# Optimization experiments

Measured on AMD Instinct MI355X. Metric: run time of the kernel, lower is better.

The kernel has to match this reference:

```python
import jax, jax.numpy as jnp
import numpy as np

N = 10000        # nodes
E = 320000       # edges (avg degree 32)
K = 3            # TAGConv default hops
D_IN, D_H, D_OUT = 256, 128, 64


def setup_inputs() -> dict:
    key = jax.random.key(0)
    ks = jax.random.split(key, 12)
    def w(k, shape):
        # xavier-uniform-ish init
        fan_in, fan_out = shape[-2], shape[-1]
        lim = float(np.sqrt(6.0 / (fan_in + fan_out)))
        return jax.random.uniform(k, shape, jnp.float32, -lim, lim)
    return {
        "x": jax.random.normal(ks[0], (N, D_IN), dtype=jnp.float32),
        "edge_index": jax.random.randint(ks[1], (2, E), 0, N, dtype=jnp.int32),
        "W1": w(ks[2], (K + 1, D_IN, D_H)),  "b1": jnp.zeros((D_H,), jnp.float32),
        "W2": w(ks[3], (K + 1, D_H, D_H)),   "b2": jnp.zeros((D_H,), jnp.float32),
        "W3": w(ks[4], (K + 1, D_H, D_OUT)), "b3": jnp.zeros((D_OUT,), jnp.float32),
        "Wf": w(ks[5], (D_OUT, D_OUT)),      "bf": jnp.zeros((D_OUT,), jnp.float32),
        "Wd": w(ks[6], (D_OUT, D_OUT)),
    }


def _gcn_norm(src, dst, n_nodes):
    # TAGConv's gcn_norm without self-loops: D^-1/2 A D^-1/2 edge weights
    deg = jax.ops.segment_sum(jnp.ones(src.shape, jnp.float32), dst,
                              num_segments=n_nodes)
    dis = jnp.where(deg > 0, jax.lax.rsqrt(jnp.maximum(deg, 1.0)), 0.0)
    return dis[src] * dis[dst]  # [E]


def _tagconv(x, src, dst, norm, W, b):
    # out = sum_{k=0..K} (A_hat^k x) @ W[k] + b
    out = x @ W[0]
    h = x
    for k in range(1, W.shape[0]):
        # message = norm_e * h[src_e], aggregated at dst
        h = jax.ops.segment_sum(norm[:, None] * h[src], dst,
                                num_segments=x.shape[0])
        out = out + h @ W[k]
    return out + b


def reference(x, edge_index, W1, b1, W2, b2, W3, b3, Wf, bf, Wd):
    src, dst = edge_index[0], edge_index[1]
    norm = _gcn_norm(src, dst, x.shape[0])
    h = jax.nn.relu(_tagconv(x, src, dst, norm, W1, b1))
    h = jax.nn.relu(_tagconv(h, src, dst, norm, W2, b2))
    h = jax.nn.relu(_tagconv(h, src, dst, norm, W3, b3))
    z = h @ Wf + bf                     # [N, D_OUT]
    adj = (z @ Wd) @ z.T                # [N, N] bilinear decode
    return adj
```

## Files before the change

### kernel.cpp

```cpp
#include <hip/hip_runtime.h>
#include <hip/hip_bf16.h>
#include <cstdint>
#include <cstddef>


typedef __attribute__((ext_vector_type(8)))  short short8;
typedef __attribute__((ext_vector_type(4)))  float f32x4;
typedef __attribute__((ext_vector_type(16))) float f32x16;

static __device__ __forceinline__ ushort f2bf(float f) {
    __hip_bfloat16 h = __float2bfloat16(f);
    return *reinterpret_cast<const ushort*>(&h);
}
static __device__ __forceinline__ float bf2f(ushort u) {
    union { uint i; float f; } v; v.i = ((uint)u) << 16; return v.f;
}


__global__ void count_kernel(const int* __restrict__ dst, int* __restrict__ counts, int E) {
    int e = blockIdx.x * blockDim.x + threadIdx.x;
    if (e < E) atomicAdd(&counts[dst[e]], 1);
}

__global__ void scan_kernel(const int* __restrict__ counts, int* __restrict__ rowstart,
                            float* __restrict__ dis, int n) {
    __shared__ int sums[1024];
    int t = threadIdx.x;
    int chunk = (n + 1023) / 1024;
    int base = t * chunk;
    int s = 0;
    for (int i = 0; i < chunk; ++i) {
        int idx = base + i;
        if (idx < n) s += counts[idx];
    }
    sums[t] = s;
    __syncthreads();
    for (int off = 1; off < 1024; off <<= 1) {
        int v = (t >= off) ? sums[t - off] : 0;
        __syncthreads();
        sums[t] += v;
        __syncthreads();
    }
    int run = sums[t] - s;
    for (int i = 0; i < chunk; ++i) {
        int idx = base + i;
        if (idx < n) {
            rowstart[idx] = run;
            int c = counts[idx];
            dis[idx] = (c > 0) ? rsqrtf((float)c) : 0.f;
            run += c;
        }
    }
    if (t == 1023) rowstart[n] = sums[1023];
}

__global__ void csr_fill_kernel(const int* __restrict__ src, const int* __restrict__ dst,
                                const float* __restrict__ dis, const int* __restrict__ rowstart,
                                int* __restrict__ cursor, int* __restrict__ csr_src,
                                float* __restrict__ csr_w, int E) {
    int e = blockIdx.x * blockDim.x + threadIdx.x;
    if (e < E) {
        int d = dst[e];
        int s = src[e];
        int pos = rowstart[d] + atomicAdd(&cursor[d], 1);
        csr_src[pos] = s;
        csr_w[pos]   = dis[s] * dis[d];
    }
}

static __device__ __forceinline__ void prep_w_elem(const float* W, ushort* Wp,
                                                   int DIN, int DOUT, int i) {
    int hp  = i / (DIN * DOUT);
    int rem = i - hp * DIN * DOUT;
    int d   = rem / DOUT;
    int o   = rem - d * DOUT;
    Wp[(size_t)(hp * DOUT + o) * DIN + d] = f2bf(W[i]);
}
static __device__ __forceinline__ void prep_wt_elem(const float* W, ushort* Wt,
                                                    int K, int C, int i) {
    int k = i / C, c = i - k * C;
    Wt[(size_t)c * K + k] = f2bf(W[i]);
}

__global__ void prep_all_kernel(const float* __restrict__ x, ushort* __restrict__ xb, int nx,
                                const float* __restrict__ W1, ushort* __restrict__ Wp1,
                                const float* __restrict__ W2, ushort* __restrict__ Wp2,
                                const float* __restrict__ W3, ushort* __restrict__ Wp3,
                                const float* __restrict__ Wf, ushort* __restrict__ Wfb,
                                const float* __restrict__ Wd, ushort* __restrict__ Wdb) {
    const int n1 = 4 * 256 * 128, n2 = 4 * 128 * 128, n3 = 4 * 128 * 64, nf = 64 * 64;
    int i = blockIdx.x * blockDim.x + threadIdx.x;
    if (i < nx) { xb[i] = f2bf(x[i]); return; }
    i -= nx;
    if (i < n1) { prep_w_elem(W1, Wp1, 256, 128, i); return; }
    i -= n1;
    if (i < n2) { prep_w_elem(W2, Wp2, 128, 128, i); return; }
    i -= n2;
    if (i < n3) { prep_w_elem(W3, Wp3, 128, 64, i); return; }
    i -= n3;
    if (i < nf) { prep_wt_elem(Wf, Wfb, 64, 64, i); return; }
    i -= nf;
    if (i < nf) { prep_wt_elem(Wd, Wdb, 64, 64, i); return; }
}

template <int DIN, int DOUT>
__global__ __launch_bounds__(256) void proj_gemm_kernel(
        const ushort* __restrict__ A, const ushort* __restrict__ Wp,
        const float* __restrict__ bias, ushort* __restrict__ y, int M) {
    constexpr int NJ = DOUT / 16;
    int tid = threadIdx.x, wave = tid >> 6, lane = tid & 63;
    int lr = lane & 15, lk = lane >> 4;
    int r0 = blockIdx.x * 32;
    int ra0 = min(r0 + lr, M - 1);
    int ra1 = min(r0 + 16 + lr, M - 1);

    f32x4 acc[2][NJ];
    #pragma unroll
    for (int mi = 0; mi < 2; ++mi)
        #pragma unroll
        for (int nj = 0; nj < NJ; ++nj)
            acc[mi][nj] = (f32x4){0.f, 0.f, 0.f, 0.f};

    const ushort* a0p = A + (size_t)ra0 * DIN + lk * 8;
    const ushort* a1p = A + (size_t)ra1 * DIN + lk * 8;
    #pragma unroll
    for (int kc = 0; kc < DIN; kc += 32) {
        short8 a0 = *(const short8*)(a0p + kc);
        short8 a1 = *(const short8*)(a1p + kc);
        #pragma unroll
        for (int nj = 0; nj < NJ; ++nj) {
            short8 b = *(const short8*)(Wp + (size_t)(wave * DOUT + nj * 16 + lr) * DIN
                                        + kc + lk * 8);
            acc[0][nj] = __builtin_amdgcn_mfma_f32_16x16x32_bf16(a0, b, acc[0][nj], 0, 0, 0);
            acc[1][nj] = __builtin_amdgcn_mfma_f32_16x16x32_bf16(a1, b, acc[1][nj], 0, 0, 0);
        }
    }

    ushort* yw = y + (size_t)wave * M * DOUT;
    #pragma unroll
    for (int nj = 0; nj < NJ; ++nj) {
        int c = nj * 16 + lr;
        float bv = (wave == 0) ? bias[c] : 0.f;
        #pragma unroll
        for (int mi = 0; mi < 2; ++mi) {
            int rbase = r0 + mi * 16 + lk * 4;
            #pragma unroll
            for (int r = 0; r < 4; ++r) {
                int row = rbase + r;
                if (row < M)
                    yw[(size_t)row * DOUT + c] = f2bf(acc[mi][nj][r] + bv);
            }
        }
    }
}

template <int D, bool RELU>
__global__ __launch_bounds__(256) void agg5_kernel(
        const ushort* __restrict__ h, const ushort* __restrict__ yk,
        const int* __restrict__ rowstart, const int* __restrict__ csr_src,
        const float* __restrict__ csr_w, ushort* __restrict__ out, int Nn) {
    constexpr int LPE = D / 8;
    constexpr int EPI = 64 / LPE;
    int wave = threadIdx.x >> 6, lane = threadIdx.x & 63;
    int n = blockIdx.x * 4 + wave;
    if (n >= Nn) return;
    int sub = lane / LPE;
    int ll  = lane % LPE;
    int beg = rowstart[n], end = rowstart[n + 1];

    float acc[8];
    #pragma unroll
    for (int v = 0; v < 8; ++v) acc[v] = 0.f;

    for (int j0 = beg; j0 < end; j0 += 64) {
        int take = end - j0;
        if (take > 64) take = 64;
        int s = 0; float w = 0.f;
        if (lane < take) { s = csr_src[j0 + lane]; w = csr_w[j0 + lane]; }
        for (int i = 0; i < take; i += EPI) {
            int e = i + sub;
            float wi = __shfl(w, e);
            int   si = __shfl(s, e);
            short8 hv = *(const short8*)(h + (size_t)si * D + ll * 8);
            #pragma unroll
            for (int v = 0; v < 8; ++v)
                acc[v] = fmaf(wi, bf2f((ushort)hv[v]), acc[v]);
        }
    }
    #pragma unroll
    for (int off = LPE; off < 64; off <<= 1) {
        #pragma unroll
        for (int v = 0; v < 8; ++v) acc[v] += __shfl_xor(acc[v], off);
    }

    if (sub == 0) {
        short8 yv = *(const short8*)(yk + (size_t)n * D + ll * 8);
        short8 o;
        #pragma unroll
        for (int v = 0; v < 8; ++v) {
            float val = acc[v] + bf2f((ushort)yv[v]);
            if (RELU) val = fmaxf(val, 0.f);
            o[v] = (short)f2bf(val);
        }
        *(short8*)(out + (size_t)n * D + ll * 8) = o;
    }
}

__global__ __launch_bounds__(256) void lin64_dual_kernel(
        const ushort* __restrict__ A, const ushort* __restrict__ Wfb,
        const float* __restrict__ bias, const ushort* __restrict__ Wdb,
        ushort* __restrict__ zz, ushort* __restrict__ zw, int M) {
    __shared__ ushort zl[4][32][72];
    int tid = threadIdx.x, wave = tid >> 6, lane = tid & 63;
    int lr = lane & 15, lk = lane >> 4;
    int r0 = blockIdx.x * 128 + wave * 32;
    int ra0 = min(r0 + lr, M - 1);
    int ra1 = min(r0 + 16 + lr, M - 1);

    short8 a[2][2], b[4][2];
    #pragma unroll
    for (int kc = 0; kc < 2; ++kc) {
        a[0][kc] = *(const short8*)(A + (size_t)ra0 * 64 + kc * 32 + lk * 8);
        a[1][kc] = *(const short8*)(A + (size_t)ra1 * 64 + kc * 32 + lk * 8);
        #pragma unroll
        for (int nj = 0; nj < 4; ++nj)
            b[nj][kc] = *(const short8*)(Wfb + (size_t)(nj * 16 + lr) * 64 + kc * 32 + lk * 8);
    }
    f32x4 acc1[2][4];
    #pragma unroll
    for (int mi = 0; mi < 2; ++mi)
        #pragma unroll
        for (int nj = 0; nj < 4; ++nj) {
            acc1[mi][nj] = (f32x4){0.f, 0.f, 0.f, 0.f};
            acc1[mi][nj] = __builtin_amdgcn_mfma_f32_16x16x32_bf16(a[mi][0], b[nj][0], acc1[mi][nj], 0, 0, 0);
            acc1[mi][nj] = __builtin_amdgcn_mfma_f32_16x16x32_bf16(a[mi][1], b[nj][1], acc1[mi][nj], 0, 0, 0);
        }

    #pragma unroll
    for (int nj = 0; nj < 4; ++nj) {
        int c = nj * 16 + lr;
        float bv = bias[c];
        #pragma unroll
        for (int mi = 0; mi < 2; ++mi) {
            int rloc = mi * 16 + lk * 4;
            #pragma unroll
            for (int r = 0; r < 4; ++r) {
                ushort u = f2bf(acc1[mi][nj][r] + bv);
                zl[wave][rloc + r][c] = u;
                int row = r0 + rloc + r;
                if (row < M) zz[(size_t)row * 64 + c] = u;
            }
        }
    }
    __syncthreads();

    short8 a2[2][2], b2[4][2];
    #pragma unroll
    for (int kc = 0; kc < 2; ++kc) {
        a2[0][kc] = *(const short8*)&zl[wave][lr][kc * 32 + lk * 8];
        a2[1][kc] = *(const short8*)&zl[wave][16 + lr][kc * 32 + lk * 8];
        #pragma unroll
        for (int nj = 0; nj < 4; ++nj)
            b2[nj][kc] = *(const short8*)(Wdb + (size_t)(nj * 16 + lr) * 64 + kc * 32 + lk * 8);
    }
    f32x4 acc2[2][4];
    #pragma unroll
    for (int mi = 0; mi < 2; ++mi)
        #pragma unroll
        for (int nj = 0; nj < 4; ++nj) {
            acc2[mi][nj] = (f32x4){0.f, 0.f, 0.f, 0.f};
            acc2[mi][nj] = __builtin_amdgcn_mfma_f32_16x16x32_bf16(a2[mi][0], b2[nj][0], acc2[mi][nj], 0, 0, 0);
            acc2[mi][nj] = __builtin_amdgcn_mfma_f32_16x16x32_bf16(a2[mi][1], b2[nj][1], acc2[mi][nj], 0, 0, 0);
        }
    #pragma unroll
    for (int nj = 0; nj < 4; ++nj) {
        int c = nj * 16 + lr;
        #pragma unroll
        for (int mi = 0; mi < 2; ++mi) {
            int rbase = r0 + mi * 16 + lk * 4;
            #pragma unroll
            for (int r = 0; r < 4; ++r) {
                int row = rbase + r;
                if (row < M) zw[(size_t)row * 64 + c] = f2bf(acc2[mi][nj][r]);
            }
        }
    }
}

__global__ __launch_bounds__(256) void decode32_kernel(
        const ushort* __restrict__ ZW, const ushort* __restrict__ Z,
        float* __restrict__ out, int Nn) {
    int tid = threadIdx.x, wave = tid >> 6, lane = tid & 63;
    int wr = wave >> 1, wc = wave & 1;
    int row0 = blockIdx.y * 128 + wr * 64;
    int col0 = blockIdx.x * 128 + wc * 64;
    int lr = lane & 31, hi = lane >> 5;

    short8 a[2][4], b[2][4];
    #pragma unroll
    for (int mi = 0; mi < 2; ++mi) {
        int ra = min(row0 + mi * 32 + lr, Nn - 1);
        int rb = min(col0 + mi * 32 + lr, Nn - 1);
        const ushort* pa = ZW + (size_t)ra * 64 + hi * 8;
        const ushort* pb = Z  + (size_t)rb * 64 + hi * 8;
        #pragma unroll
        for (int kc = 0; kc < 4; ++kc) {
            a[mi][kc] = *(const short8*)(pa + kc * 16);
            b[mi][kc] = *(const short8*)(pb + kc * 16);
        }
    }

    f32x16 acc[2][2];
    #pragma unroll
    for (int mi = 0; mi < 2; ++mi)
        #pragma unroll
        for (int nj = 0; nj < 2; ++nj) {
            f32x16 c;
            #pragma unroll
            for (int q = 0; q < 16; ++q) c[q] = 0.f;
            #pragma unroll
            for (int kc = 0; kc < 4; ++kc)
                c = __builtin_amdgcn_mfma_f32_32x32x16_bf16(a[mi][kc], b[nj][kc], c, 0, 0, 0);
            acc[mi][nj] = c;
        }

    bool full = (row0 + 64 <= Nn) && (col0 + 64 <= Nn);
    #pragma unroll
    for (int mi = 0; mi < 2; ++mi)
        #pragma unroll
        for (int nj = 0; nj < 2; ++nj) {
            int cb = col0 + nj * 32 + lr;
            #pragma unroll
            for (int reg = 0; reg < 16; ++reg) {
                int row = row0 + mi * 32 + (reg & 3) + 8 * (reg >> 2) + 4 * hi;
                if (full) {
                    __builtin_nontemporal_store(acc[mi][nj][reg], &out[(size_t)row * Nn + cb]);
                } else {
                    if (row < Nn && cb < Nn)
                        __builtin_nontemporal_store(acc[mi][nj][reg], &out[(size_t)row * Nn + cb]);
                }
            }
        }
}


extern "C" void kernel_launch(void* const* d_in, const int* in_sizes, int n_in,
                              void* d_out, int out_size, void* d_ws, size_t ws_size,
                              hipStream_t stream) {
    const float* x  = (const float*)d_in[0];
    const int*   ei = (const int*)d_in[1];
    const float* W1 = (const float*)d_in[2];
    const float* b1 = (const float*)d_in[3];
    const float* W2 = (const float*)d_in[4];
    const float* b2 = (const float*)d_in[5];
    const float* W3 = (const float*)d_in[6];
    const float* b3 = (const float*)d_in[7];
    const float* Wf = (const float*)d_in[8];
    const float* bf = (const float*)d_in[9];
    const float* Wd = (const float*)d_in[10];

    const int Nn = in_sizes[0] / 256;
    const int E  = in_sizes[1] / 2;
    const int* src = ei;
    const int* dst = ei + E;

    char* p = (char*)d_ws;
    auto alloc = [&](size_t bytes) -> char* {
        char* r = p;
        p += (bytes + 255) & ~(size_t)255;
        return r;
    };
    size_t nslot = ((size_t)Nn * 4 + 255) & ~(size_t)255;
    int*    counts   = (int*)alloc((size_t)Nn * 4);
    int*    cursor   = (int*)alloc((size_t)Nn * 4);
    int*    rowstart = (int*)alloc((size_t)(Nn + 1) * 4);
    float*  dis      = (float*)alloc((size_t)Nn * 4);
    int*    csr_src  = (int*)alloc((size_t)E * 4);
    float*  csr_w    = (float*)alloc((size_t)E * 4);
    ushort* xb       = (ushort*)alloc((size_t)Nn * 256 * 2);
    ushort* yb       = (ushort*)alloc((size_t)4 * Nn * 128 * 2);
    ushort* t1       = (ushort*)alloc((size_t)Nn * 128 * 2);
    ushort* t2       = (ushort*)alloc((size_t)Nn * 128 * 2);
    ushort* out1b    = (ushort*)alloc((size_t)Nn * 128 * 2);
    ushort* out2b    = (ushort*)alloc((size_t)Nn * 128 * 2);
    ushort* out3b    = (ushort*)alloc((size_t)Nn * 64 * 2);
    ushort* zzb      = (ushort*)alloc((size_t)Nn * 64 * 2);
    ushort* zwb      = (ushort*)alloc((size_t)Nn * 64 * 2);
    ushort* Wp1      = (ushort*)alloc((size_t)512 * 256 * 2);
    ushort* Wp2      = (ushort*)alloc((size_t)512 * 128 * 2);
    ushort* Wp3      = (ushort*)alloc((size_t)256 * 128 * 2);
    ushort* Wfb      = (ushort*)alloc((size_t)64 * 64 * 2);
    ushort* Wdb      = (ushort*)alloc((size_t)64 * 64 * 2);

    hipMemsetAsync(counts, 0, nslot + (size_t)Nn * 4, stream);

    int eb = (E + 255) / 256;
    count_kernel<<<eb, 256, 0, stream>>>(dst, counts, E);
    scan_kernel<<<1, 1024, 0, stream>>>(counts, rowstart, dis, Nn);
    csr_fill_kernel<<<eb, 256, 0, stream>>>(src, dst, dis, rowstart, cursor,
                                            csr_src, csr_w, E);

    int nx = Nn * 256;
    int nprep = nx + 4 * 256 * 128 + 4 * 128 * 128 + 4 * 128 * 64 + 64 * 64 + 64 * 64;
    prep_all_kernel<<<(nprep + 255) / 256, 256, 0, stream>>>(
        x, xb, nx, W1, Wp1, W2, Wp2, W3, Wp3, Wf, Wfb, Wd, Wdb);

    int ab = (Nn + 3) / 4;
    int gb = (Nn + 31) / 32;
    size_t Y128 = (size_t)Nn * 128;
    size_t Y64  = (size_t)Nn * 64;

    proj_gemm_kernel<256, 128><<<gb, 256, 0, stream>>>(xb, Wp1, b1, yb, Nn);
    agg5_kernel<128, false><<<ab, 256, 0, stream>>>(yb + 3 * Y128, yb + 2 * Y128,
                                                    rowstart, csr_src, csr_w, t1, Nn);
    agg5_kernel<128, false><<<ab, 256, 0, stream>>>(t1, yb + 1 * Y128,
                                                    rowstart, csr_src, csr_w, t2, Nn);
    agg5_kernel<128, true ><<<ab, 256, 0, stream>>>(t2, yb,
                                                    rowstart, csr_src, csr_w, out1b, Nn);

    proj_gemm_kernel<128, 128><<<gb, 256, 0, stream>>>(out1b, Wp2, b2, yb, Nn);
    agg5_kernel<128, false><<<ab, 256, 0, stream>>>(yb + 3 * Y128, yb + 2 * Y128,
                                                    rowstart, csr_src, csr_w, t1, Nn);
    agg5_kernel<128, false><<<ab, 256, 0, stream>>>(t1, yb + 1 * Y128,
                                                    rowstart, csr_src, csr_w, t2, Nn);
    agg5_kernel<128, true ><<<ab, 256, 0, stream>>>(t2, yb,
                                                    rowstart, csr_src, csr_w, out2b, Nn);

    proj_gemm_kernel<128, 64><<<gb, 256, 0, stream>>>(out2b, Wp3, b3, yb, Nn);
    agg5_kernel<64, false><<<ab, 256, 0, stream>>>(yb + 3 * Y64, yb + 2 * Y64,
                                                   rowstart, csr_src, csr_w, t1, Nn);
    agg5_kernel<64, false><<<ab, 256, 0, stream>>>(t1, yb + 1 * Y64,
                                                   rowstart, csr_src, csr_w, t2, Nn);
    agg5_kernel<64, true ><<<ab, 256, 0, stream>>>(t2, yb,
                                                   rowstart, csr_src, csr_w, out3b, Nn);

    int lb = (Nn + 127) / 128;
    lin64_dual_kernel<<<lb, 256, 0, stream>>>(out3b, Wfb, bf, Wdb, zzb, zwb, Nn);

    int db = (Nn + 127) / 128;
    decode32_kernel<<<dim3(db, db), 256, 0, stream>>>(zwb, zzb, (float*)d_out, Nn);
}
```

Measured before the change: 332.3 us.

## Merge setup kernels, pack CSR edges as int2, prefetch gathers in aggregation

Folds the degree-count pass into the x/weight prep kernel, which now converts x to bf16 with float4 loads, removing one launch. The CSR source index and edge weight are stored together as one int2, so each edge needs a single 8-byte load. The aggregation kernel software-pipelines the neighbour-row gather, issuing the next short8 load before consuming the current one. Blocks grow from 4 to 8 waves (512 threads). The padded trip count relies on zero-weight lanes reading row 0, and the larger blocks may change occupancy.

New measurement: 324.0 us. 1.03x faster.

```diff
diff --git a/kernel.cpp b/kernel.cpp
--- a/kernel.cpp
+++ b/kernel.cpp
@@ -17,9 +17,47 @@
 }
 
 
-__global__ void count_kernel(const int* __restrict__ dst, int* __restrict__ counts, int E) {
-    int e = blockIdx.x * blockDim.x + threadIdx.x;
-    if (e < E) atomicAdd(&counts[dst[e]], 1);
+static __device__ __forceinline__ void prep_w_elem(const float* W, ushort* Wp,
+                                                   int DIN, int DOUT, int i) {
+    int hp  = i / (DIN * DOUT);
+    int rem = i - hp * DIN * DOUT;
+    int d   = rem / DOUT;
+    int o   = rem - d * DOUT;
+    Wp[(size_t)(hp * DOUT + o) * DIN + d] = f2bf(W[i]);
+}
+static __device__ __forceinline__ void prep_wt_elem(const float* W, ushort* Wt,
+                                                    int K, int C, int i) {
+    int k = i / C, c = i - k * C;
+    Wt[(size_t)c * K + k] = f2bf(W[i]);
+}
+
+__global__ void setup_kernel(const int* __restrict__ dst, int* __restrict__ counts, int E,
+                             const float* __restrict__ x, ushort* __restrict__ xb, int nx4,
+                             const float* __restrict__ W1, ushort* __restrict__ Wp1,
+                             const float* __restrict__ W2, ushort* __restrict__ Wp2,
+                             const float* __restrict__ W3, ushort* __restrict__ Wp3,
+                             const float* __restrict__ Wf, ushort* __restrict__ Wfb,
+                             const float* __restrict__ Wd, ushort* __restrict__ Wdb) {
+    const int n1 = 4 * 256 * 128, n2 = 4 * 128 * 128, n3 = 4 * 128 * 64, nf = 64 * 64;
+    int i = blockIdx.x * blockDim.x + threadIdx.x;
+    if (i < E) atomicAdd(&counts[dst[i]], 1);
+    if (i < nx4) {
+        float4 v = ((const float4*)x)[i];
+        ushort4 o;
+        o.x = f2bf(v.x); o.y = f2bf(v.y); o.z = f2bf(v.z); o.w = f2bf(v.w);
+        ((ushort4*)xb)[i] = o;
+        return;
+    }
+    int j = i - nx4;
+    if (j < n1) { prep_w_elem(W1, Wp1, 256, 128, j); return; }
+    j -= n1;
+    if (j < n2) { prep_w_elem(W2, Wp2, 128, 128, j); return; }
+    j -= n2;
+    if (j < n3) { prep_w_elem(W3, Wp3, 128, 64, j); return; }
+    j -= n3;
+    if (j < nf) { prep_wt_elem(Wf, Wfb, 64, 64, j); return; }
+    j -= nf;
+    if (j < nf) { prep_wt_elem(Wd, Wdb, 64, 64, j); return; }
 }
 
 __global__ void scan_kernel(const int* __restrict__ counts, int* __restrict__ rowstart,
@@ -56,51 +94,14 @@
 
 __global__ void csr_fill_kernel(const int* __restrict__ src, const int* __restrict__ dst,
                                 const float* __restrict__ dis, const int* __restrict__ rowstart,
-                                int* __restrict__ cursor, int* __restrict__ csr_src,
-                                float* __restrict__ csr_w, int E) {
+                                int* __restrict__ cursor, int2* __restrict__ csr2, int E) {
     int e = blockIdx.x * blockDim.x + threadIdx.x;
     if (e < E) {
         int d = dst[e];
         int s = src[e];
         int pos = rowstart[d] + atomicAdd(&cursor[d], 1);
-        csr_src[pos] = s;
-        csr_w[pos]   = dis[s] * dis[d];
-    }
-}
-
-static __device__ __forceinline__ void prep_w_elem(const float* W, ushort* Wp,
-                                                   int DIN, int DOUT, int i) {
-    int hp  = i / (DIN * DOUT);
-    int rem = i - hp * DIN * DOUT;
-    int d   = rem / DOUT;
-    int o   = rem - d * DOUT;
-    Wp[(size_t)(hp * DOUT + o) * DIN + d] = f2bf(W[i]);
-}
-static __device__ __forceinline__ void prep_wt_elem(const float* W, ushort* Wt,
-                                                    int K, int C, int i) {
-    int k = i / C, c = i - k * C;
-    Wt[(size_t)c * K + k] = f2bf(W[i]);
-}
-
-__global__ void prep_all_kernel(const float* __restrict__ x, ushort* __restrict__ xb, int nx,
-                                const float* __restrict__ W1, ushort* __restrict__ Wp1,
-                                const float* __restrict__ W2, ushort* __restrict__ Wp2,
-                                const float* __restrict__ W3, ushort* __restrict__ Wp3,
-                                const float* __restrict__ Wf, ushort* __restrict__ Wfb,
-                                const float* __restrict__ Wd, ushort* __restrict__ Wdb) {
-    const int n1 = 4 * 256 * 128, n2 = 4 * 128 * 128, n3 = 4 * 128 * 64, nf = 64 * 64;
-    int i = blockIdx.x * blockDim.x + threadIdx.x;
-    if (i < nx) { xb[i] = f2bf(x[i]); return; }
-    i -= nx;
-    if (i < n1) { prep_w_elem(W1, Wp1, 256, 128, i); return; }
-    i -= n1;
-    if (i < n2) { prep_w_elem(W2, Wp2, 128, 128, i); return; }
-    i -= n2;
-    if (i < n3) { prep_w_elem(W3, Wp3, 128, 64, i); return; }
-    i -= n3;
-    if (i < nf) { prep_wt_elem(Wf, Wfb, 64, 64, i); return; }
-    i -= nf;
-    if (i < nf) { prep_wt_elem(Wd, Wdb, 64, 64, i); return; }
+        csr2[pos] = make_int2(s, __float_as_int(dis[s] * dis[d]));
+    }
 }
 
 template <int DIN, int DOUT>
@@ -155,14 +156,14 @@
 }
 
 template <int D, bool RELU>
-__global__ __launch_bounds__(256) void agg5_kernel(
+__global__ __launch_bounds__(512) void agg6_kernel(
         const ushort* __restrict__ h, const ushort* __restrict__ yk,
-        const int* __restrict__ rowstart, const int* __restrict__ csr_src,
-        const float* __restrict__ csr_w, ushort* __restrict__ out, int Nn) {
+        const int* __restrict__ rowstart, const int2* __restrict__ csr2,
+        ushort* __restrict__ out, int Nn) {
     constexpr int LPE = D / 8;
     constexpr int EPI = 64 / LPE;
     int wave = threadIdx.x >> 6, lane = threadIdx.x & 63;
-    int n = blockIdx.x * 4 + wave;
+    int n = blockIdx.x * 8 + wave;
     if (n >= Nn) return;
     int sub = lane / LPE;
     int ll  = lane % LPE;
@@ -175,18 +176,29 @@
     for (int j0 = beg; j0 < end; j0 += 64) {
         int take = end - j0;
         if (take > 64) take = 64;
-        int s = 0; float w = 0.f;
-        if (lane < take) { s = csr_src[j0 + lane]; w = csr_w[j0 + lane]; }
-        for (int i = 0; i < take; i += EPI) {
-            int e = i + sub;
-            float wi = __shfl(w, e);
-            int   si = __shfl(s, e);
-            short8 hv = *(const short8*)(h + (size_t)si * D + ll * 8);
+        int2 ed = make_int2(0, 0);
+        if (lane < take) ed = csr2[j0 + lane];
+        int   s = ed.x;
+        float w = __int_as_float(ed.y);
+        int tt = (take + EPI - 1) & ~(EPI - 1);
+
+        float wc = __shfl(w, sub);
+        int   sc = __shfl(s, sub);
+        short8 hv = *(const short8*)(h + (size_t)sc * D + ll * 8);
+        for (int i = EPI; i < tt; i += EPI) {
+            float wn = __shfl(w, i + sub);
+            int   sn = __shfl(s, i + sub);
+            short8 hn = *(const short8*)(h + (size_t)sn * D + ll * 8);
             #pragma unroll
             for (int v = 0; v < 8; ++v)
-                acc[v] = fmaf(wi, bf2f((ushort)hv[v]), acc[v]);
-        }
-    }
+                acc[v] = fmaf(wc, bf2f((ushort)hv[v]), acc[v]);
+            wc = wn; hv = hn;
+        }
+        #pragma unroll
+        for (int v = 0; v < 8; ++v)
+            acc[v] = fmaf(wc, bf2f((ushort)hv[v]), acc[v]);
+    }
+
     #pragma unroll
     for (int off = LPE; off < 64; off <<= 1) {
         #pragma unroll
@@ -375,8 +387,7 @@
     int*    cursor   = (int*)alloc((size_t)Nn * 4);
     int*    rowstart = (int*)alloc((size_t)(Nn + 1) * 4);
     float*  dis      = (float*)alloc((size_t)Nn * 4);
-    int*    csr_src  = (int*)alloc((size_t)E * 4);
-    float*  csr_w    = (float*)alloc((size_t)E * 4);
+    int2*   csr2     = (int2*)alloc((size_t)E * 8);
     ushort* xb       = (ushort*)alloc((size_t)Nn * 256 * 2);
     ushort* yb       = (ushort*)alloc((size_t)4 * Nn * 128 * 2);
     ushort* t1       = (ushort*)alloc((size_t)Nn * 128 * 2);
@@ -394,45 +405,46 @@
 
     hipMemsetAsync(counts, 0, nslot + (size_t)Nn * 4, stream);
 
+    int nx4 = Nn * 256 / 4;
+    int nprep = nx4 + 4 * 256 * 128 + 4 * 128 * 128 + 4 * 128 * 64 + 64 * 64 + 64 * 64;
+    int nsetup = nprep > E ? nprep : E;
+    setup_kernel<<<(nsetup + 255) / 256, 256, 0, stream>>>(
+        dst, counts, E, x, xb, nx4,
+        W1, Wp1, W2, Wp2, W3, Wp3, Wf, Wfb, Wd, Wdb);
+
+    scan_kernel<<<1, 1024, 0, stream>>>(counts, rowstart, dis, Nn);
+
     int eb = (E + 255) / 256;
-    count_kernel<<<eb, 256, 0, stream>>>(dst, counts, E);
-    scan_kernel<<<1, 1024, 0, stream>>>(counts, rowstart, dis, Nn);
-    csr_fill_kernel<<<eb, 256, 0, stream>>>(src, dst, dis, rowstart, cursor,
-                                            csr_src, csr_w, E);
-
-    int nx = Nn * 256;
-    int nprep = nx + 4 * 256 * 128 + 4 * 128 * 128 + 4 * 128 * 64 + 64 * 64 + 64 * 64;
-    prep_all_kernel<<<(nprep + 255) / 256, 256, 0, stream>>>(
-        x, xb, nx, W1, Wp1, W2, Wp2, W3, Wp3, Wf, Wfb, Wd, Wdb);
-
-    int ab = (Nn + 3) / 4;
+    csr_fill_kernel<<<eb, 256, 0, stream>>>(src, dst, dis, rowstart, cursor, csr2, E);
+
+    int ab = (Nn + 7) / 8;
     int gb = (Nn + 31) / 32;
     size_t Y128 = (size_t)Nn * 128;
     size_t Y64  = (size_t)Nn * 64;
 
     proj_gemm_kernel<256, 128><<<gb, 256, 0, stream>>>(xb, Wp1, b1, yb, Nn);
-    agg5_kernel<128, false><<<ab, 256, 0, stream>>>(yb + 3 * Y128, yb + 2 * Y128,
-                                                    rowstart, csr_src, csr_w, t1, Nn);
-    agg5_kernel<128, false><<<ab, 256, 0, stream>>>(t1, yb + 1 * Y128,
-                                                    rowstart, csr_src, csr_w, t2, Nn);
-    agg5_kernel<128, true ><<<ab, 256, 0, stream>>>(t2, yb,
-                                                    rowstart, csr_src, csr_w, out1b, Nn);
+    agg6_kernel<128, false><<<ab, 512, 0, stream>>>(yb + 3 * Y128, yb + 2 * Y128,
+                                                    rowstart, csr2, t1, Nn);
+    agg6_kernel<128, false><<<ab, 512, 0, stream>>>(t1, yb + 1 * Y128,
+                                                    rowstart, csr2, t2, Nn);
+    agg6_kernel<128, true ><<<ab, 512, 0, stream>>>(t2, yb,
+                                                    rowstart, csr2, out1b, Nn);
 
     proj_gemm_kernel<128, 128><<<gb, 256, 0, stream>>>(out1b, Wp2, b2, yb, Nn);
-    agg5_kernel<128, false><<<ab, 256, 0, stream>>>(yb + 3 * Y128, yb + 2 * Y128,
-                                                    rowstart, csr_src, csr_w, t1, Nn);
-    agg5_kernel<128, false><<<ab, 256, 0, stream>>>(t1, yb + 1 * Y128,
-                                                    rowstart, csr_src, csr_w, t2, Nn);
-    agg5_kernel<128, true ><<<ab, 256, 0, stream>>>(t2, yb,
-                                                    rowstart, csr_src, csr_w, out2b, Nn);
+    agg6_kernel<128, false><<<ab, 512, 0, stream>>>(yb + 3 * Y128, yb + 2 * Y128,
+                                                    rowstart, csr2, t1, Nn);
+    agg6_kernel<128, false><<<ab, 512, 0, stream>>>(t1, yb + 1 * Y128,
+                                                    rowstart, csr2, t2, Nn);
+    agg6_kernel<128, true ><<<ab, 512, 0, stream>>>(t2, yb,
+                                                    rowstart, csr2, out2b, Nn);
 
     proj_gemm_kernel<128, 64><<<gb, 256, 0, stream>>>(out2b, Wp3, b3, yb, Nn);
-    agg5_kernel<64, false><<<ab, 256, 0, stream>>>(yb + 3 * Y64, yb + 2 * Y64,
-                                                   rowstart, csr_src, csr_w, t1, Nn);
-    agg5_kernel<64, false><<<ab, 256, 0, stream>>>(t1, yb + 1 * Y64,
-                                                   rowstart, csr_src, csr_w, t2, Nn);
-    agg5_kernel<64, true ><<<ab, 256, 0, stream>>>(t2, yb,
-                                                   rowstart, csr_src, csr_w, out3b, Nn);
+    agg6_kernel<64, false><<<ab, 512, 0, stream>>>(yb + 3 * Y64, yb + 2 * Y64,
+                                                   rowstart, csr2, t1, Nn);
+    agg6_kernel<64, false><<<ab, 512, 0, stream>>>(t1, yb + 1 * Y64,
+                                                   rowstart, csr2, t2, Nn);
+    agg6_kernel<64, true ><<<ab, 512, 0, stream>>>(t2, yb,
+                                                   rowstart, csr2, out3b, Nn);
 
     int lb = (Nn + 127) / 128;
     lin64_dual_kernel<<<lb, 256, 0, stream>>>(out3b, Wfb, bf, Wdb, zzb, zwb, Nn);
```
